# Performance work log

Hardware: AMD Instinct MI355X
Metric: run time of the kernel (lower is better)

Reference implementation:

```python
import jax, jax.numpy as jnp
import numpy as np

EPS = 1e-6
NUM_HEADS = 16

def _ln(x):
    # LayerNorm32, no affine, eps=1e-6, computed in fp32
    x32 = x.astype(jnp.float32)
    mu = jnp.mean(x32, axis=-1, keepdims=True)
    var = jnp.var(x32, axis=-1, keepdims=True)
    return ((x32 - mu) * jax.lax.rsqrt(var + EPS)).astype(x.dtype)

def _mha(q, k, v):
    # q,k,v: [B, L, H, D]
    d = q.shape[-1]
    scale = 1.0 / jnp.sqrt(jnp.asarray(d, q.dtype))
    s = jnp.einsum('bqhd,bkhd->bhqk', q, k) * scale
    p = jax.nn.softmax(s, axis=-1)
    o = jnp.einsum('bhqk,bkhd->bqhd', p, v)
    return o.reshape(o.shape[0], o.shape[1], -1)

def setup_inputs() -> dict:
    key = jax.random.key(0)
    ks = jax.random.split(key, 10)
    B, L, C, Lc, Cc = 4, 2048, 1024, 1024, 1024
    Dff = 4 * C
    s = 0.02
    return {
        'x': jax.random.normal(ks[0], (B, L, C), jnp.float32),
        'context': jax.random.normal(ks[1], (B, Lc, Cc), jnp.float32),
        'w_qkv': jax.random.normal(ks[2], (C, 3 * C), jnp.float32) * s,
        'b_qkv': jnp.zeros((3 * C,), jnp.float32),
        'w_os': jax.random.normal(ks[3], (C, C), jnp.float32) * s,
        'b_os': jnp.zeros((C,), jnp.float32),
        'w_qc': jax.random.normal(ks[4], (C, C), jnp.float32) * s,
        'b_qc': jnp.zeros((C,), jnp.float32),
        'w_kvc': jax.random.normal(ks[5], (Cc, 2 * C), jnp.float32) * s,
        'b_kvc': jnp.zeros((2 * C,), jnp.float32),
        'w_oc': jax.random.normal(ks[6], (C, C), jnp.float32) * s,
        'b_oc': jnp.zeros((C,), jnp.float32),
        'w_fc1': jax.random.normal(ks[7], (C, Dff), jnp.float32) * s,
        'b_fc1': jnp.zeros((Dff,), jnp.float32),
        'w_fc2': jax.random.normal(ks[8], (Dff, C), jnp.float32) * s,
        'b_fc2': jnp.zeros((C,), jnp.float32),
    }

def reference(x, context, w_qkv, b_qkv, w_os, b_os, w_qc, b_qc, w_kvc, b_kvc,
              w_oc, b_oc, w_fc1, b_fc1, w_fc2, b_fc2):
    B, L, C = x.shape
    H = NUM_HEADS
    D = C // H
    # --- self attention (pre-norm, full) ---
    h = _ln(x)
    qkv = (h @ w_qkv + b_qkv).reshape(B, L, 3, H, D)
    q, k, v = qkv[:, :, 0], qkv[:, :, 1], qkv[:, :, 2]
    h = _mha(q, k, v) @ w_os + b_os
    x = x + h
    # --- cross attention ---
    h = _ln(x)
    q = (h @ w_qc + b_qc).reshape(B, L, H, D)
    Lc = context.shape[1]
    kv = (context @ w_kvc + b_kvc).reshape(B, Lc, 2, H, D)
    k, v = kv[:, :, 0], kv[:, :, 1]
    h = _mha(q, k, v) @ w_oc + b_oc
    x = x + h
    # --- sparse FFN (GELU tanh) ---
    h = _ln(x)
    h = jax.nn.gelu(h @ w_fc1 + b_fc1, approximate=True) @ w_fc2 + b_fc2
    return x + h
```

## Files before the change

kernel.cpp:

```cpp
#include <hip/hip_runtime.h>

typedef unsigned short ushort_t;
typedef __attribute__((ext_vector_type(8))) short short8;
typedef __attribute__((ext_vector_type(4))) float f32x4;
typedef __attribute__((ext_vector_type(4))) unsigned short ushort4v;

__device__ inline ushort_t f2bf(float f) {
    union { float f; unsigned u; } v; v.f = f;
    return (ushort_t)((v.u + 0x7FFFu + ((v.u >> 16) & 1u)) >> 16);
}
__device__ inline float bf2f(ushort_t u) {
    union { unsigned u; float f; } v; v.u = ((unsigned)u) << 16;
    return v.f;
}

__device__ inline float fast_exp2(float x) {
#if __has_builtin(__builtin_amdgcn_exp2f)
    return __builtin_amdgcn_exp2f(x);
#else
    float r; asm("v_exp_f32 %0, %1" : "=v"(r) : "v"(x)); return r;
#endif
}

__device__ inline void gld16(const ushort_t* g, ushort_t* l) {
    __builtin_amdgcn_global_load_lds(
        (const __attribute__((address_space(1))) unsigned int*)g,
        (__attribute__((address_space(3))) unsigned int*)l, 16, 0, 0);
}

__device__ inline int xcd_swz(int id, int nwg) {
    int q = nwg >> 3;
    return (id & 7) * q + (id >> 3);
}

struct WPrep {
    const float* src[7];
    ushort_t*    dst[7];
    int K[7], N[7];
    int tilesBefore[8];
};

__global__ void w_prep_all(WPrep P) {
    __shared__ float t[64][65];
    const int bid = blockIdx.x;
    int e = 0;
#pragma unroll
    for (int i = 0; i < 7; i++) if (bid >= P.tilesBefore[i + 1]) e = i + 1;
    const int lt = bid - P.tilesBefore[e];
    const int K = P.K[e], N = P.N[e];
    const int ntx = N >> 6;
    const int n0 = (lt % ntx) * 64, k0 = (lt / ntx) * 64;
    const float* w = P.src[e];
    ushort_t* out = P.dst[e];
    const int tid = threadIdx.x;
#pragma unroll
    for (int i = 0; i < 16; i++) {
        int idx = tid + i * 256;
        int r = idx >> 6, c = idx & 63;
        t[r][c] = w[(size_t)(k0 + r) * N + n0 + c];
    }
    __syncthreads();
#pragma unroll
    for (int i = 0; i < 16; i++) {
        int idx = tid + i * 256;
        int nr = idx >> 6, kc = idx & 63;
        out[(size_t)(n0 + nr) * K + k0 + kc] = f2bf(t[kc][nr]);
    }
}

__global__ void v_transpose(const ushort_t* __restrict__ V, int vStride, int rowsPerBatch,
                            ushort_t* __restrict__ Vt, int Lk) {
    __shared__ __align__(16) ushort_t t[64][72];
    const int bh = blockIdx.y, k0 = blockIdx.x * 64;
    const int b = bh >> 4, h = bh & 15;
    const int tid = threadIdx.x;
    const ushort_t* src = V + (size_t)(b * rowsPerBatch + k0) * vStride + h * 64;
#pragma unroll
    for (int i = 0; i < 2; i++) {
        int ch = tid + i * 256;
        int r = ch >> 3, c = (ch & 7) * 8;
        *(short8*)(&t[r][c]) = *(const short8*)(src + (size_t)r * vStride + c);
    }
    __syncthreads();
#pragma unroll
    for (int i = 0; i < 2; i++) {
        int ch = tid + i * 256;
        int d = ch >> 3, c = (ch & 7) * 8;
        short8 o;
#pragma unroll
        for (int j = 0; j < 8; j++) o[j] = (short)t[c + j][d];
        *(short8*)(Vt + ((size_t)bh * 64 + d) * Lk + k0 + c) = o;
    }
}

__global__ void f32_to_bf16_vec(const float* __restrict__ in, ushort_t* __restrict__ out, int n4) {
    int i = blockIdx.x * blockDim.x + threadIdx.x;
    if (i < n4) {
        float4 v = ((const float4*)in)[i];
        ushort4v o;
        o[0] = f2bf(v.x); o[1] = f2bf(v.y); o[2] = f2bf(v.z); o[3] = f2bf(v.w);
        ((ushort4v*)out)[i] = o;
    }
}

__global__ void ln_rows(const float* __restrict__ in, ushort_t* __restrict__ out) {
    __shared__ float s1[4], s2[4];
    const int row = blockIdx.x;
    const int tid = threadIdx.x;
    const float4 v = ((const float4*)(in + (size_t)row * 1024))[tid];
    float s  = v.x + v.y + v.z + v.w;
    float ss = v.x * v.x + v.y * v.y + v.z * v.z + v.w * v.w;
#pragma unroll
    for (int d = 32; d >= 1; d >>= 1) {
        s  += __shfl_down(s, d, 64);
        ss += __shfl_down(ss, d, 64);
    }
    if ((tid & 63) == 0) { s1[tid >> 6] = s; s2[tid >> 6] = ss; }
    __syncthreads();
    float sum = s1[0] + s1[1] + s1[2] + s1[3];
    float sqs = s2[0] + s2[1] + s2[2] + s2[3];
    float mu  = sum * (1.0f / 1024.0f);
    float var = sqs * (1.0f / 1024.0f) - mu * mu;
    float rs  = rsqrtf(var + 1e-6f);
    ushort4v o;
    o[0] = f2bf((v.x - mu) * rs);
    o[1] = f2bf((v.y - mu) * rs);
    o[2] = f2bf((v.z - mu) * rs);
    o[3] = f2bf((v.w - mu) * rs);
    ((ushort4v*)(out + (size_t)row * 1024))[tid] = o;
}

#define EPI_BF16 0
#define EPI_GELU 1
#define EPI_RES  2

template <int EPI>
__global__ void gemm_bt(const ushort_t* __restrict__ A, const ushort_t* __restrict__ Bt,
                        const float* __restrict__ bias, const float* __restrict__ res,
                        void* __restrict__ outp, int M, int N, int K) {
    __shared__ __align__(16) ushort_t As[128 * 64];
    __shared__ __align__(16) ushort_t Bs[128 * 64];
    const int tid = threadIdx.x;
    const int lane = tid & 63, wave = tid >> 6;
    const int nwg = gridDim.x * gridDim.y;
    const int sid = xcd_swz(blockIdx.y * gridDim.x + blockIdx.x, nwg);
    const int m0 = (sid / gridDim.x) * 128, n0 = (sid % gridDim.x) * 128;
    const int wr = (wave >> 1) * 64, wc = (wave & 1) * 64;
    const int lr = lane & 15, lg = lane >> 4;

    f32x4 acc[4][4];
#pragma unroll
    for (int i = 0; i < 4; i++)
#pragma unroll
        for (int j = 0; j < 4; j++) acc[i][j] = f32x4{0.f, 0.f, 0.f, 0.f};

    for (int k0 = 0; k0 < K; k0 += 64) {
#pragma unroll
        for (int i = 0; i < 4; i++) {
            int ch = tid + i * 256;
            int r = ch >> 3;
            int kcs = (((ch & 7) ^ (r & 7))) * 8;
            gld16(A  + (size_t)(m0 + r) * K + k0 + kcs, As + ch * 8);
            gld16(Bt + (size_t)(n0 + r) * K + k0 + kcs, Bs + ch * 8);
        }
        __syncthreads();
#pragma unroll
        for (int ks = 0; ks < 2; ks++) {
            short8 af[4], bfr[4];
#pragma unroll
            for (int m = 0; m < 4; m++) {
                int r = wr + m * 16 + lr;
                int kc = ks * 4 + lg;
                af[m] = *(const short8*)(As + r * 64 + ((kc ^ (r & 7)) << 3));
            }
#pragma unroll
            for (int n = 0; n < 4; n++) {
                int r = wc + n * 16 + lr;
                int kc = ks * 4 + lg;
                bfr[n] = *(const short8*)(Bs + r * 64 + ((kc ^ (r & 7)) << 3));
            }
#pragma unroll
            for (int m = 0; m < 4; m++)
#pragma unroll
                for (int n = 0; n < 4; n++)
                    acc[m][n] = __builtin_amdgcn_mfma_f32_16x16x32_bf16(af[m], bfr[n], acc[m][n], 0, 0, 0);
        }
        __syncthreads();
    }

#pragma unroll
    for (int m = 0; m < 4; m++) {
        int rowb = m0 + wr + m * 16 + lg * 4;
#pragma unroll
        for (int n = 0; n < 4; n++) {
            int col = n0 + wc + n * 16 + lr;
            float bcol = bias[col];
            f32x4 v = acc[m][n];
#pragma unroll
            for (int q = 0; q < 4; q++) {
                float x = v[q] + bcol;
                if (EPI == EPI_GELU) {
                    float u = 0.7978845608028654f * (x + 0.044715f * x * x * x);
                    float a = fabsf(u);
                    float tt = fast_exp2(-2.885390081777927f * a);
                    float th = copysignf((1.0f - tt) / (1.0f + tt), u);
                    x = 0.5f * x * (1.0f + th);
                }
                size_t off = (size_t)(rowb + q) * N + col;
                if (EPI == EPI_RES) ((float*)outp)[off] = x + res[off];
                else                ((ushort_t*)outp)[off] = f2bf(x);
            }
        }
    }
}

__global__ __launch_bounds__(512, 2)
void attn_fwd(const ushort_t* __restrict__ Q, int qStride,
              const ushort_t* __restrict__ Kp, int kvStride, int kvBatchRows,
              const ushort_t* __restrict__ Vt, int Lk,
              ushort_t* __restrict__ O) {
    __shared__ __align__(16) ushort_t Ks[2][64 * 64];
    __shared__ __align__(16) ushort_t Vts[2][64 * 64];
    __shared__ __align__(16) ushort_t Ps[8][16 * 64];
    const int tid = threadIdx.x, lane = tid & 63, wave = tid >> 6;
    const int lr = lane & 15, lg = lane >> 4;
    const int sid = xcd_swz(blockIdx.x, gridDim.x);
    const int qb = sid & 15, h = (sid >> 4) & 15, b = sid >> 8;
    const int qRow0 = b * 2048 + qb * 128;
    const int kvRow0 = b * kvBatchRows;
    const int hc = h * 64;
    const ushort_t* vt_base = Vt + (size_t)(b * 16 + h) * 64 * Lk;

    short8 qf[2];
    {
        const ushort_t* qrow = Q + (size_t)(qRow0 + wave * 16 + lr) * qStride + hc;
        short8 r0 = *(const short8*)(qrow + lg * 8);
        short8 r1 = *(const short8*)(qrow + 32 + lg * 8);
        const float s = 0.125f * 1.4426950408889634f;
#pragma unroll
        for (int j = 0; j < 8; j++) {
            qf[0][j] = (short)f2bf(bf2f((ushort_t)r0[j]) * s);
            qf[1][j] = (short)f2bf(bf2f((ushort_t)r1[j]) * s);
        }
    }

    f32x4 oacc[4];
#pragma unroll
    for (int d = 0; d < 4; d++) oacc[d] = f32x4{0.f, 0.f, 0.f, 0.f};
    float mrun = -1e30f, lrun = 0.f;

    const int nt = Lk >> 6;

    auto stage = [&](int buf, int kt) {
        int r = tid >> 3;
        int kcs = (((tid & 7) ^ (r & 7))) * 8;
        gld16(Kp + (size_t)(kvRow0 + kt + r) * kvStride + hc + kcs, Ks[buf] + tid * 8);
        gld16(vt_base + (size_t)r * Lk + kt + kcs, Vts[buf] + tid * 8);
    };

    stage(0, 0);
    __syncthreads();
    int cur = 0;

    for (int t = 0; t < nt; ++t) {
        if (t + 1 < nt) stage(cur ^ 1, (t + 1) * 64);

        const ushort_t* Kc = Ks[cur];
        const ushort_t* Vc = Vts[cur];

        f32x4 sacc[4];
        __builtin_amdgcn_s_setprio(1);
#pragma unroll
        for (int n = 0; n < 4; n++) {
            int r = n * 16 + lr;
            short8 k0 = *(const short8*)(Kc + r * 64 + ((lg ^ (r & 7)) << 3));
            short8 k1 = *(const short8*)(Kc + r * 64 + (((4 + lg) ^ (r & 7)) << 3));
            f32x4 s = f32x4{0.f, 0.f, 0.f, 0.f};
            s = __builtin_amdgcn_mfma_f32_16x16x32_bf16(k0, qf[0], s, 0, 0, 0);
            s = __builtin_amdgcn_mfma_f32_16x16x32_bf16(k1, qf[1], s, 0, 0, 0);
            sacc[n] = s;
        }
        __builtin_amdgcn_s_setprio(0);

        float mx = sacc[0][0];
#pragma unroll
        for (int n = 0; n < 4; n++)
#pragma unroll
            for (int r = 0; r < 4; r++) if (n | r) mx = fmaxf(mx, sacc[n][r]);
        mx = fmaxf(mx, __shfl_xor(mx, 16, 64));
        mx = fmaxf(mx, __shfl_xor(mx, 32, 64));

        if (!__all(mx <= mrun + 11.5416f)) {
            float mnew = fmaxf(mrun, mx);
            float al = fast_exp2(mrun - mnew);
            float a0 = __shfl(al, lg * 4 + 0, 64);
            float a1 = __shfl(al, lg * 4 + 1, 64);
            float a2 = __shfl(al, lg * 4 + 2, 64);
            float a3 = __shfl(al, lg * 4 + 3, 64);
#pragma unroll
            for (int dn = 0; dn < 4; dn++) {
                oacc[dn][0] *= a0; oacc[dn][1] *= a1;
                oacc[dn][2] *= a2; oacc[dn][3] *= a3;
            }
            lrun *= al;
            mrun = mnew;
        }

        float rsum = 0.f;
#pragma unroll
        for (int n = 0; n < 4; n++)
#pragma unroll
            for (int r = 0; r < 4; r++) {
                float p = fast_exp2(sacc[n][r] - mrun);
                sacc[n][r] = p;
                rsum += p;
            }
        rsum += __shfl_xor(rsum, 16, 64);
        rsum += __shfl_xor(rsum, 32, 64);
        lrun += rsum;

        ushort_t* Pw = &Ps[wave][0];
#pragma unroll
        for (int n = 0; n < 4; n++) {
            unsigned w0, w1;
            asm("v_cvt_pk_bf16_f32 %0, %1, %2" : "=v"(w0) : "v"(sacc[n][0]), "v"(sacc[n][1]));
            asm("v_cvt_pk_bf16_f32 %0, %1, %2" : "=v"(w1) : "v"(sacc[n][2]), "v"(sacc[n][3]));
            int kc = n * 2 + (lg >> 1);
            uint2 u; u.x = w0; u.y = w1;
            *(uint2*)((char*)Pw + lr * 128 + ((kc ^ (lr & 7)) << 4) + (lg & 1) * 8) = u;
        }

        short8 pf0 = *(const short8*)(Pw + lr * 64 + ((lg ^ (lr & 7)) << 3));
        short8 pf1 = *(const short8*)(Pw + lr * 64 + (((4 + lg) ^ (lr & 7)) << 3));
        __builtin_amdgcn_s_setprio(1);
#pragma unroll
        for (int dn = 0; dn < 4; dn++) {
            int r = dn * 16 + lr;
            short8 v0 = *(const short8*)(Vc + r * 64 + ((lg ^ (r & 7)) << 3));
            short8 v1 = *(const short8*)(Vc + r * 64 + (((4 + lg) ^ (r & 7)) << 3));
            oacc[dn] = __builtin_amdgcn_mfma_f32_16x16x32_bf16(pf0, v0, oacc[dn], 0, 0, 0);
            oacc[dn] = __builtin_amdgcn_mfma_f32_16x16x32_bf16(pf1, v1, oacc[dn], 0, 0, 0);
        }
        __builtin_amdgcn_s_setprio(0);
        __syncthreads();
        cur ^= 1;
    }

    float linv[4];
#pragma unroll
    for (int r = 0; r < 4; r++) linv[r] = 1.0f / __shfl(lrun, lg * 4 + r, 64);

#pragma unroll
    for (int dn = 0; dn < 4; dn++)
#pragma unroll
        for (int q = 0; q < 4; q++) {
            float o = oacc[dn][q] * linv[q];
            int row = qRow0 + wave * 16 + lg * 4 + q;
            int col = hc + dn * 16 + lr;
            O[(size_t)row * 1024 + col] = f2bf(o);
        }
}

extern "C" void kernel_launch(void* const* d_in, const int* in_sizes, int n_in,
                              void* d_out, int out_size, void* d_ws, size_t ws_size,
                              hipStream_t stream) {
    const float* x     = (const float*)d_in[0];
    const float* ctx   = (const float*)d_in[1];
    const float* w_qkv = (const float*)d_in[2];
    const float* b_qkv = (const float*)d_in[3];
    const float* w_os  = (const float*)d_in[4];
    const float* b_os  = (const float*)d_in[5];
    const float* w_qc  = (const float*)d_in[6];
    const float* b_qc  = (const float*)d_in[7];
    const float* w_kvc = (const float*)d_in[8];
    const float* b_kvc = (const float*)d_in[9];
    const float* w_oc  = (const float*)d_in[10];
    const float* b_oc  = (const float*)d_in[11];
    const float* w_fc1 = (const float*)d_in[12];
    const float* b_fc1 = (const float*)d_in[13];
    const float* w_fc2 = (const float*)d_in[14];
    const float* b_fc2 = (const float*)d_in[15];
    float* out = (float*)d_out;

    char* ws = (char*)d_ws;
    ushort_t* wqkvT = (ushort_t*)(ws + 0);
    ushort_t* wosT  = (ushort_t*)(ws + 6291456);
    ushort_t* wqcT  = (ushort_t*)(ws + 8388608);
    ushort_t* wkvcT = (ushort_t*)(ws + 10485760);
    ushort_t* wocT  = (ushort_t*)(ws + 14680064);
    ushort_t* wfc1T = (ushort_t*)(ws + 16777216);
    ushort_t* wfc2T = (ushort_t*)(ws + 25165824);
    ushort_t* qkv_bf  = (ushort_t*)(ws + 33554432);
    ushort_t* q_bf    = (ushort_t*)(ws + 33554432);
    ushort_t* kv_bf   = (ushort_t*)(ws + 50331648);
    ushort_t* vt_c    = (ushort_t*)(ws + 67108864);
    ushort_t* ffn_bf  = (ushort_t*)(ws + 33554432);
    ushort_t* ctx_bf  = (ushort_t*)(ws + 83886080);
    ushort_t* attn_bf = (ushort_t*)(ws + 92274688);
    ushort_t* h_bf    = (ushort_t*)(ws + 109051904);
    ushort_t* vt_s    = (ushort_t*)(ws + 109051904);

    const dim3 tb(256);
    const dim3 tb512(512);

    WPrep P;
    P.src[0] = w_qkv; P.dst[0] = wqkvT; P.K[0] = 1024; P.N[0] = 3072;
    P.src[1] = w_os;  P.dst[1] = wosT;  P.K[1] = 1024; P.N[1] = 1024;
    P.src[2] = w_qc;  P.dst[2] = wqcT;  P.K[2] = 1024; P.N[2] = 1024;
    P.src[3] = w_kvc; P.dst[3] = wkvcT; P.K[3] = 1024; P.N[3] = 2048;
    P.src[4] = w_oc;  P.dst[4] = wocT;  P.K[4] = 1024; P.N[4] = 1024;
    P.src[5] = w_fc1; P.dst[5] = wfc1T; P.K[5] = 1024; P.N[5] = 4096;
    P.src[6] = w_fc2; P.dst[6] = wfc2T; P.K[6] = 4096; P.N[6] = 1024;
    P.tilesBefore[0] = 0;
    for (int i = 0; i < 7; i++)
        P.tilesBefore[i + 1] = P.tilesBefore[i] + (P.N[i] / 64) * (P.K[i] / 64);
    w_prep_all<<<dim3(P.tilesBefore[7]), tb, 0, stream>>>(P);
    f32_to_bf16_vec<<<4096, tb, 0, stream>>>(ctx, ctx_bf, 1048576);

    ln_rows<<<8192, tb, 0, stream>>>(x, h_bf);
    gemm_bt<EPI_BF16><<<dim3(24, 64), tb, 0, stream>>>(h_bf, wqkvT, b_qkv, nullptr, qkv_bf, 8192, 3072, 1024);
    v_transpose<<<dim3(32, 64), tb, 0, stream>>>(qkv_bf + 2048, 3072, 2048, vt_s, 2048);
    attn_fwd<<<dim3(1024), tb512, 0, stream>>>(qkv_bf, 3072, qkv_bf + 1024, 3072, 2048,
                                               vt_s, 2048, attn_bf);
    gemm_bt<EPI_RES><<<dim3(8, 64), tb, 0, stream>>>(attn_bf, wosT, b_os, x, out, 8192, 1024, 1024);

    ln_rows<<<8192, tb, 0, stream>>>(out, h_bf);
    gemm_bt<EPI_BF16><<<dim3(8, 64), tb, 0, stream>>>(h_bf, wqcT, b_qc, nullptr, q_bf, 8192, 1024, 1024);
    gemm_bt<EPI_BF16><<<dim3(16, 32), tb, 0, stream>>>(ctx_bf, wkvcT, b_kvc, nullptr, kv_bf, 4096, 2048, 1024);
    v_transpose<<<dim3(16, 64), tb, 0, stream>>>(kv_bf + 1024, 2048, 1024, vt_c, 1024);
    attn_fwd<<<dim3(1024), tb512, 0, stream>>>(q_bf, 1024, kv_bf, 2048, 1024,
                                               vt_c, 1024, attn_bf);
    gemm_bt<EPI_RES><<<dim3(8, 64), tb, 0, stream>>>(attn_bf, wocT, b_oc, out, out, 8192, 1024, 1024);

    ln_rows<<<8192, tb, 0, stream>>>(out, h_bf);
    gemm_bt<EPI_GELU><<<dim3(32, 64), tb, 0, stream>>>(h_bf, wfc1T, b_fc1, nullptr, ffn_bf, 8192, 4096, 1024);
    gemm_bt<EPI_RES><<<dim3(8, 64), tb, 0, stream>>>(ffn_bf, wfc2T, b_fc2, out, out, 8192, 1024, 4096);
}
```

Measured before the change: 569.0 us.

## Process two 16-row query tiles per wave in attention to reuse K/V fragments

Each wave now handles 32 query rows (two 16-row sub-tiles) instead of 16, so each block covers 256 query rows and the grid is halved to 512 blocks. K and V fragments loaded from LDS are reused across both sub-tiles, which halves K/V global staging and LDS reads per unit of work and gives more independent MFMAs to interleave. The cost is roughly double the accumulator and score registers per thread, which may hurt occupancy under launch bounds of 2 blocks, and fewer blocks (512 over 256 CUs) can cause tail imbalance.

New measurement: 548.2 us. -3.6%, faster.

```diff
diff --git a/kernel.cpp b/kernel.cpp
--- a/kernel.cpp
+++ b/kernel.cpp
@@ -221,33 +221,36 @@
               ushort_t* __restrict__ O) {
     __shared__ __align__(16) ushort_t Ks[2][64 * 64];
     __shared__ __align__(16) ushort_t Vts[2][64 * 64];
-    __shared__ __align__(16) ushort_t Ps[8][16 * 64];
+    __shared__ __align__(16) ushort_t Ps[8][2][16 * 64];
     const int tid = threadIdx.x, lane = tid & 63, wave = tid >> 6;
     const int lr = lane & 15, lg = lane >> 4;
     const int sid = xcd_swz(blockIdx.x, gridDim.x);
-    const int qb = sid & 15, h = (sid >> 4) & 15, b = sid >> 8;
-    const int qRow0 = b * 2048 + qb * 128;
+    const int qb = sid & 7, h = (sid >> 3) & 15, b = sid >> 7;
+    const int qRow0 = b * 2048 + qb * 256;
     const int kvRow0 = b * kvBatchRows;
     const int hc = h * 64;
     const ushort_t* vt_base = Vt + (size_t)(b * 16 + h) * 64 * Lk;
 
-    short8 qf[2];
-    {
-        const ushort_t* qrow = Q + (size_t)(qRow0 + wave * 16 + lr) * qStride + hc;
+    short8 qf[2][2];
+#pragma unroll
+    for (int qh = 0; qh < 2; qh++) {
+        const ushort_t* qrow = Q + (size_t)(qRow0 + wave * 32 + qh * 16 + lr) * qStride + hc;
         short8 r0 = *(const short8*)(qrow + lg * 8);
         short8 r1 = *(const short8*)(qrow + 32 + lg * 8);
         const float s = 0.125f * 1.4426950408889634f;
 #pragma unroll
         for (int j = 0; j < 8; j++) {
-            qf[0][j] = (short)f2bf(bf2f((ushort_t)r0[j]) * s);
-            qf[1][j] = (short)f2bf(bf2f((ushort_t)r1[j]) * s);
-        }
-    }
-
-    f32x4 oacc[4];
-#pragma unroll
-    for (int d = 0; d < 4; d++) oacc[d] = f32x4{0.f, 0.f, 0.f, 0.f};
-    float mrun = -1e30f, lrun = 0.f;
+            qf[qh][0][j] = (short)f2bf(bf2f((ushort_t)r0[j]) * s);
+            qf[qh][1][j] = (short)f2bf(bf2f((ushort_t)r1[j]) * s);
+        }
+    }
+
+    f32x4 oacc[2][4];
+#pragma unroll
+    for (int qh = 0; qh < 2; qh++)
+#pragma unroll
+        for (int d = 0; d < 4; d++) oacc[qh][d] = f32x4{0.f, 0.f, 0.f, 0.f};
+    float mrun[2] = {-1e30f, -1e30f}, lrun[2] = {0.f, 0.f};
 
     const int nt = Lk >> 6;
 
@@ -268,97 +271,113 @@
         const ushort_t* Kc = Ks[cur];
         const ushort_t* Vc = Vts[cur];
 
-        f32x4 sacc[4];
+        f32x4 sacc[2][4];
         __builtin_amdgcn_s_setprio(1);
 #pragma unroll
         for (int n = 0; n < 4; n++) {
             int r = n * 16 + lr;
             short8 k0 = *(const short8*)(Kc + r * 64 + ((lg ^ (r & 7)) << 3));
             short8 k1 = *(const short8*)(Kc + r * 64 + (((4 + lg) ^ (r & 7)) << 3));
-            f32x4 s = f32x4{0.f, 0.f, 0.f, 0.f};
-            s = __builtin_amdgcn_mfma_f32_16x16x32_bf16(k0, qf[0], s, 0, 0, 0);
-            s = __builtin_amdgcn_mfma_f32_16x16x32_bf16(k1, qf[1], s, 0, 0, 0);
-            sacc[n] = s;
+#pragma unroll
+            for (int qh = 0; qh < 2; qh++) {
+                f32x4 s = f32x4{0.f, 0.f, 0.f, 0.f};
+                s = __builtin_amdgcn_mfma_f32_16x16x32_bf16(k0, qf[qh][0], s, 0, 0, 0);
+                s = __builtin_amdgcn_mfma_f32_16x16x32_bf16(k1, qf[qh][1], s, 0, 0, 0);
+                sacc[qh][n] = s;
+            }
         }
         __builtin_amdgcn_s_setprio(0);
 
-        float mx = sacc[0][0];
-#pragma unroll
-        for (int n = 0; n < 4; n++)
-#pragma unroll
-            for (int r = 0; r < 4; r++) if (n | r) mx = fmaxf(mx, sacc[n][r]);
-        mx = fmaxf(mx, __shfl_xor(mx, 16, 64));
-        mx = fmaxf(mx, __shfl_xor(mx, 32, 64));
-
-        if (!__all(mx <= mrun + 11.5416f)) {
-            float mnew = fmaxf(mrun, mx);
-            float al = fast_exp2(mrun - mnew);
-            float a0 = __shfl(al, lg * 4 + 0, 64);
-            float a1 = __shfl(al, lg * 4 + 1, 64);
-            float a2 = __shfl(al, lg * 4 + 2, 64);
-            float a3 = __shfl(al, lg * 4 + 3, 64);
-#pragma unroll
-            for (int dn = 0; dn < 4; dn++) {
-                oacc[dn][0] *= a0; oacc[dn][1] *= a1;
-                oacc[dn][2] *= a2; oacc[dn][3] *= a3;
-            }
-            lrun *= al;
-            mrun = mnew;
-        }
-
-        float rsum = 0.f;
-#pragma unroll
-        for (int n = 0; n < 4; n++)
-#pragma unroll
-            for (int r = 0; r < 4; r++) {
-                float p = fast_exp2(sacc[n][r] - mrun);
-                sacc[n][r] = p;
-                rsum += p;
-            }
-        rsum += __shfl_xor(rsum, 16, 64);
-        rsum += __shfl_xor(rsum, 32, 64);
-        lrun += rsum;
-
-        ushort_t* Pw = &Ps[wave][0];
-#pragma unroll
-        for (int n = 0; n < 4; n++) {
-            unsigned w0, w1;
-            asm("v_cvt_pk_bf16_f32 %0, %1, %2" : "=v"(w0) : "v"(sacc[n][0]), "v"(sacc[n][1]));
-            asm("v_cvt_pk_bf16_f32 %0, %1, %2" : "=v"(w1) : "v"(sacc[n][2]), "v"(sacc[n][3]));
-            int kc = n * 2 + (lg >> 1);
-            uint2 u; u.x = w0; u.y = w1;
-            *(uint2*)((char*)Pw + lr * 128 + ((kc ^ (lr & 7)) << 4) + (lg & 1) * 8) = u;
-        }
-
-        short8 pf0 = *(const short8*)(Pw + lr * 64 + ((lg ^ (lr & 7)) << 3));
-        short8 pf1 = *(const short8*)(Pw + lr * 64 + (((4 + lg) ^ (lr & 7)) << 3));
+#pragma unroll
+        for (int qh = 0; qh < 2; qh++) {
+            float mx = sacc[qh][0][0];
+#pragma unroll
+            for (int n = 0; n < 4; n++)
+#pragma unroll
+                for (int r = 0; r < 4; r++) if (n | r) mx = fmaxf(mx, sacc[qh][n][r]);
+            mx = fmaxf(mx, __shfl_xor(mx, 16, 64));
+            mx = fmaxf(mx, __shfl_xor(mx, 32, 64));
+
+            if (!__all(mx <= mrun[qh] + 11.5416f)) {
+                float mnew = fmaxf(mrun[qh], mx);
+                float al = fast_exp2(mrun[qh] - mnew);
+                float a0 = __shfl(al, lg * 4 + 0, 64);
+                float a1 = __shfl(al, lg * 4 + 1, 64);
+                float a2 = __shfl(al, lg * 4 + 2, 64);
+                float a3 = __shfl(al, lg * 4 + 3, 64);
+#pragma unroll
+                for (int dn = 0; dn < 4; dn++) {
+                    oacc[qh][dn][0] *= a0; oacc[qh][dn][1] *= a1;
+                    oacc[qh][dn][2] *= a2; oacc[qh][dn][3] *= a3;
+                }
+                lrun[qh] *= al;
+                mrun[qh] = mnew;
+            }
+
+            float rsum = 0.f;
+#pragma unroll
+            for (int n = 0; n < 4; n++)
+#pragma unroll
+                for (int r = 0; r < 4; r++) {
+                    float p = fast_exp2(sacc[qh][n][r] - mrun[qh]);
+                    sacc[qh][n][r] = p;
+                    rsum += p;
+                }
+            rsum += __shfl_xor(rsum, 16, 64);
+            rsum += __shfl_xor(rsum, 32, 64);
+            lrun[qh] += rsum;
+
+            ushort_t* Pw = &Ps[wave][qh][0];
+#pragma unroll
+            for (int n = 0; n < 4; n++) {
+                unsigned w0, w1;
+                asm("v_cvt_pk_bf16_f32 %0, %1, %2" : "=v"(w0) : "v"(sacc[qh][n][0]), "v"(sacc[qh][n][1]));
+                asm("v_cvt_pk_bf16_f32 %0, %1, %2" : "=v"(w1) : "v"(sacc[qh][n][2]), "v"(sacc[qh][n][3]));
+                int kc = n * 2 + (lg >> 1);
+                uint2 u; u.x = w0; u.y = w1;
+                *(uint2*)((char*)Pw + lr * 128 + ((kc ^ (lr & 7)) << 4) + (lg & 1) * 8) = u;
+            }
+        }
+
+        short8 pf[2][2];
+#pragma unroll
+        for (int qh = 0; qh < 2; qh++) {
+            const ushort_t* Pw = &Ps[wave][qh][0];
+            pf[qh][0] = *(const short8*)(Pw + lr * 64 + ((lg ^ (lr & 7)) << 3));
+            pf[qh][1] = *(const short8*)(Pw + lr * 64 + (((4 + lg) ^ (lr & 7)) << 3));
+        }
         __builtin_amdgcn_s_setprio(1);
 #pragma unroll
         for (int dn = 0; dn < 4; dn++) {
             int r = dn * 16 + lr;
             short8 v0 = *(const short8*)(Vc + r * 64 + ((lg ^ (r & 7)) << 3));
             short8 v1 = *(const short8*)(Vc + r * 64 + (((4 + lg) ^ (r & 7)) << 3));
-            oacc[dn] = __builtin_amdgcn_mfma_f32_16x16x32_bf16(pf0, v0, oacc[dn], 0, 0, 0);
-            oacc[dn] = __builtin_amdgcn_mfma_f32_16x16x32_bf16(pf1, v1, oacc[dn], 0, 0, 0);
+#pragma unroll
+            for (int qh = 0; qh < 2; qh++) {
+                oacc[qh][dn] = __builtin_amdgcn_mfma_f32_16x16x32_bf16(pf[qh][0], v0, oacc[qh][dn], 0, 0, 0);
+                oacc[qh][dn] = __builtin_amdgcn_mfma_f32_16x16x32_bf16(pf[qh][1], v1, oacc[qh][dn], 0, 0, 0);
+            }
         }
         __builtin_amdgcn_s_setprio(0);
         __syncthreads();
         cur ^= 1;
     }
 
-    float linv[4];
-#pragma unroll
-    for (int r = 0; r < 4; r++) linv[r] = 1.0f / __shfl(lrun, lg * 4 + r, 64);
-
-#pragma unroll
-    for (int dn = 0; dn < 4; dn++)
-#pragma unroll
-        for (int q = 0; q < 4; q++) {
-            float o = oacc[dn][q] * linv[q];
-            int row = qRow0 + wave * 16 + lg * 4 + q;
-            int col = hc + dn * 16 + lr;
-            O[(size_t)row * 1024 + col] = f2bf(o);
-        }
+#pragma unroll
+    for (int qh = 0; qh < 2; qh++) {
+        float linv[4];
+#pragma unroll
+        for (int r = 0; r < 4; r++) linv[r] = 1.0f / __shfl(lrun[qh], lg * 4 + r, 64);
+#pragma unroll
+        for (int dn = 0; dn < 4; dn++)
+#pragma unroll
+            for (int q = 0; q < 4; q++) {
+                float o = oacc[qh][dn][q] * linv[q];
+                int row = qRow0 + wave * 32 + qh * 16 + lg * 4 + q;
+                int col = hc + dn * 16 + lr;
+                O[(size_t)row * 1024 + col] = f2bf(o);
+            }
+    }
 }
 
 extern "C" void kernel_launch(void* const* d_in, const int* in_sizes, int n_in,
@@ -420,16 +439,16 @@
     ln_rows<<<8192, tb, 0, stream>>>(x, h_bf);
     gemm_bt<EPI_BF16><<<dim3(24, 64), tb, 0, stream>>>(h_bf, wqkvT, b_qkv, nullptr, qkv_bf, 8192, 3072, 1024);
     v_transpose<<<dim3(32, 64), tb, 0, stream>>>(qkv_bf + 2048, 3072, 2048, vt_s, 2048);
-    attn_fwd<<<dim3(1024), tb512, 0, stream>>>(qkv_bf, 3072, qkv_bf + 1024, 3072, 2048,
-                                               vt_s, 2048, attn_bf);
+    attn_fwd<<<dim3(512), tb512, 0, stream>>>(qkv_bf, 3072, qkv_bf + 1024, 3072, 2048,
+                                              vt_s, 2048, attn_bf);
     gemm_bt<EPI_RES><<<dim3(8, 64), tb, 0, stream>>>(attn_bf, wosT, b_os, x, out, 8192, 1024, 1024);
 
     ln_rows<<<8192, tb, 0, stream>>>(out, h_bf);
     gemm_bt<EPI_BF16><<<dim3(8, 64), tb, 0, stream>>>(h_bf, wqcT, b_qc, nullptr, q_bf, 8192, 1024, 1024);
     gemm_bt<EPI_BF16><<<dim3(16, 32), tb, 0, stream>>>(ctx_bf, wkvcT, b_kvc, nullptr, kv_bf, 4096, 2048, 1024);
     v_transpose<<<dim3(16, 64), tb, 0, stream>>>(kv_bf + 1024, 2048, 1024, vt_c, 1024);
-    attn_fwd<<<dim3(1024), tb512, 0, stream>>>(q_bf, 1024, kv_bf, 2048, 1024,
-                                               vt_c, 1024, attn_bf);
+    attn_fwd<<<dim3(512), tb512, 0, stream>>>(q_bf, 1024, kv_bf, 2048, 1024,
+                                              vt_c, 1024, attn_bf);
     gemm_bt<EPI_RES><<<dim3(8, 64), tb, 0, stream>>>(attn_bf, wocT, b_oc, out, out, 8192, 1024, 1024);
 
     ln_rows<<<8192, tb, 0, stream>>>(out, h_bf);
```
